# Optimization experiments

Hardware: AMD Instinct MI355X
Metric: run time of the kernel (lower is better)

The kernel has to match this reference:

```python
import jax, jax.numpy as jnp
import numpy as np
import math

LEVELS = 256
DISTANCES = [1, 3, 5, 7]
ANGLES_DEG = [0, 45, 90, 135]


def _offsets():
    # offset_row = round(sin(theta)*d), offset_col = round(cos(theta)*d)
    offs = []
    for d in DISTANCES:
        row = []
        for theta in ANGLES_DEG:
            rad = theta * math.pi / 180.0
            orow = int(np.round(np.sin(rad) * d))
            ocol = int(np.round(np.cos(rad) * d))
            row.append((orow, ocol))
        offs.append(row)
    return offs


def _glcm_contrast(q, orow, ocol, rows, cols):
    # q: (H, W) int32 quantized image in [0, LEVELS-1]
    sr = 0 if orow > 0 else -orow
    er = rows - orow if orow > 0 else rows
    sc = 0 if ocol > 0 else -ocol
    ec = cols - ocol if ocol > 0 else cols
    a = q[sr:er, sc:ec]
    b = q[sr + orow:er + orow, sc + ocol:ec + ocol]
    idx = (a * LEVELS + b).ravel()
    # scatter-add co-occurrence histogram (the irregular-access core)
    hist = jnp.zeros((LEVELS * LEVELS,), jnp.float32).at[idx].add(1.0)
    P = hist.reshape(LEVELS, LEVELS)
    P = P + P.T                      # symmetric
    s = P.sum()
    P = P / jnp.where(s == 0, 1.0, s)  # normalize
    lv = jnp.arange(LEVELS, dtype=jnp.float32)
    diff2 = (lv[:, None] - lv[None, :]) ** 2
    return (diff2 * P).sum()         # Haralick contrast


def setup_inputs() -> dict:
    key = jax.random.key(0)
    x = jax.random.normal(key, (32, 1, 1024, 1024), dtype=jnp.float32)
    return {"x": x}


def reference(x):
    B, C, H, W = x.shape
    img = x[:, 0]  # (B, H, W), single channel
    # per-image rescale to [0, LEVELS-1] then truncate to int (matches int() cast)
    mn = img.min(axis=(1, 2), keepdims=True)
    mx = img.max(axis=(1, 2), keepdims=True)
    q = ((LEVELS - 1) * (img - mn) / (mx - mn)).astype(jnp.int32)
    q = jax.lax.stop_gradient(q)
    offs = _offsets()
    rows_out = []
    for d_row in offs:
        cols_out = []
        for (orow, ocol) in d_row:
            f = lambda qi, o=orow, c=ocol: _glcm_contrast(qi, o, c, H, W)
            cols_out.append(jax.vmap(f)(q))  # (B,)
        rows_out.append(jnp.stack(cols_out, axis=-1))  # (B, n_angles)
    out = jnp.stack(rows_out, axis=-2)  # (B, n_dist, n_angles)
    return out[:, None, :, :]  # (B, 1, 4, 4)
```

## Files before the change

kernel.cpp:

```cpp
#include <hip/hip_runtime.h>

#define H 1024
#define W 1024
#define NIMG 32
#define NOFF 16
#define NACC 17
#define TH 32
#define TW 256
#define TROWS 39
#define TSTR 304

__device__ __forceinline__ int sdot4i(unsigned a, unsigned b, int c) {
#if __has_builtin(__builtin_amdgcn_sdot4)
    return __builtin_amdgcn_sdot4((int)a, (int)b, c, false);
#else
    c += (int)(signed char)(a)       * (int)(signed char)(b);
    c += (int)(signed char)(a >> 8)  * (int)(signed char)(b >> 8);
    c += (int)(signed char)(a >> 16) * (int)(signed char)(b >> 16);
    c += (int)(signed char)(a >> 24) * (int)(signed char)(b >> 24);
    return c;
#endif
}

__device__ __forceinline__ unsigned funnel(unsigned hi, unsigned lo, int shiftBytes) {
#if __has_builtin(__builtin_amdgcn_alignbit)
    return __builtin_amdgcn_alignbit(hi, lo, shiftBytes * 8);
#else
    unsigned long long pair = (((unsigned long long)hi) << 32) | lo;
    return (unsigned)(pair >> (shiftBytes * 8));
#endif
}

__device__ __forceinline__ int wave_sum(int v) {
    v += __builtin_amdgcn_update_dpp(0, v, 0x111, 0xf, 0xf, false);
    v += __builtin_amdgcn_update_dpp(0, v, 0x112, 0xf, 0xf, false);
    v += __builtin_amdgcn_update_dpp(0, v, 0x114, 0xf, 0xf, false);
    v += __builtin_amdgcn_update_dpp(0, v, 0x118, 0xf, 0xf, false);
    v += __builtin_amdgcn_update_dpp(0, v, 0x142, 0xa, 0xf, false);
    v += __builtin_amdgcn_update_dpp(0, v, 0x143, 0xc, 0xf, false);
    return v;
}

template <int OC>
__device__ __forceinline__ int dot8(const unsigned* w, const unsigned* aw, int acc) {
#pragma unroll
    for (int m = 0; m < 8; ++m) {
        const int S = 16 + 4 * m + OC;
        unsigned b;
        if ((S & 3) == 0) b = w[S >> 2];
        else              b = funnel(w[(S >> 2) + 1], w[S >> 2], S & 3);
        acc = sdot4i(aw[m], b, acc);
    }
    return acc;
}

__device__ __forceinline__ void load16w(const unsigned char* wp, unsigned* w) {
    uint4 t0 = *(const uint4*)(wp);
    uint4 t1 = *(const uint4*)(wp + 16);
    uint4 t2 = *(const uint4*)(wp + 32);
    uint4 t3 = *(const uint4*)(wp + 48);
    w[0] = t0.x;  w[1] = t0.y;  w[2] = t0.z;  w[3] = t0.w;
    w[4] = t1.x;  w[5] = t1.y;  w[6] = t1.z;  w[7] = t1.w;
    w[8] = t2.x;  w[9] = t2.y;  w[10] = t2.z; w[11] = t2.w;
    w[12] = t3.x; w[13] = t3.y; w[14] = t3.z; w[15] = t3.w;
}

__device__ __forceinline__ void load8mid(const unsigned char* wp, unsigned* w) {
    uint4 t1 = *(const uint4*)(wp + 16);
    uint4 t2 = *(const uint4*)(wp + 32);
    w[4] = t1.x;  w[5] = t1.y;  w[6] = t1.z;  w[7] = t1.w;
    w[8] = t2.x;  w[9] = t2.y;  w[10] = t2.z; w[11] = t2.w;
}

__device__ __forceinline__ unsigned pack4(float4 f, float s, float b) {
    unsigned q0 = (unsigned)(int)fmaf(f.x, s, b);
    unsigned q1 = (unsigned)(int)fmaf(f.y, s, b);
    unsigned q2 = (unsigned)(int)fmaf(f.z, s, b);
    unsigned q3 = (unsigned)(int)fmaf(f.w, s, b);
    return (((q0 & 255u)) | ((q1 & 255u) << 8) | ((q2 & 255u) << 16) | ((q3 & 255u) << 24)) ^ 0x80808080u;
}

__global__ __launch_bounds__(256)
void minmax_partial(const float* __restrict__ x, float* __restrict__ pmn,
                    float* __restrict__ pmx, unsigned long long* __restrict__ gacc,
                    int* __restrict__ RowS, int* __restrict__ ColS) {
    int img = blockIdx.y;
    int chunk = blockIdx.x;
    int tid = threadIdx.x;
    if (chunk == 0) {
        if (tid < NACC) gacc[img * NACC + tid] = 0ull;
        if (tid >= 32 && tid < 46) RowS[img * 14 + tid - 32] = 0;
        if (tid >= 64 && tid < 78) ColS[img * 14 + tid - 64] = 0;
    }
    const float4* b4 = (const float4*)(x + (size_t)img * (H * (size_t)W) +
                                       (size_t)chunk * (H * W / 64));
    float mn = INFINITY, mx = -INFINITY;
    for (int i = tid; i < 4096; i += 256) {
        float4 v = b4[i];
        mn = fminf(mn, fminf(fminf(v.x, v.y), fminf(v.z, v.w)));
        mx = fmaxf(mx, fmaxf(fmaxf(v.x, v.y), fmaxf(v.z, v.w)));
    }
    for (int o = 32; o > 0; o >>= 1) {
        mn = fminf(mn, __shfl_down(mn, o, 64));
        mx = fmaxf(mx, __shfl_down(mx, o, 64));
    }
    __shared__ float smn[4], smx[4];
    int wave = tid >> 6, lane = tid & 63;
    if (lane == 0) { smn[wave] = mn; smx[wave] = mx; }
    __syncthreads();
    if (tid == 0) {
        mn = fminf(fminf(smn[0], smn[1]), fminf(smn[2], smn[3]));
        mx = fmaxf(fmaxf(smx[0], smx[1]), fmaxf(smx[2], smx[3]));
        pmn[img * 64 + chunk] = mn;
        pmx[img * 64 + chunk] = mx;
    }
}

__global__ __launch_bounds__(256)
void glcm_main(const float* __restrict__ x, const float* __restrict__ pmn,
               const float* __restrict__ pmx, unsigned long long* __restrict__ gacc,
               int* __restrict__ RowS, int* __restrict__ ColS,
               short* __restrict__ cornerWS) {
    __shared__ __align__(16) unsigned char tile[TROWS * TSTR];
    __shared__ int wsum[4][NACC];
    __shared__ int sRB[7], sCB[7];
    __shared__ float sms[2];
    int tid = threadIdx.x;
    int img = blockIdx.z;
    int gr0 = blockIdx.y * TH;
    int gc0 = blockIdx.x * TW;

    if (tid < 64) {
        float mn = pmn[img * 64 + tid], mx = pmx[img * 64 + tid];
        for (int o = 32; o > 0; o >>= 1) {
            mn = fminf(mn, __shfl_down(mn, o, 64));
            mx = fmaxf(mx, __shfl_down(mx, o, 64));
        }
        if (tid == 0) {
            float sc = 255.0f / (mx - mn);
            sms[0] = sc; sms[1] = -mn * sc;
        }
    }
    if (tid >= 64 && tid < 71) { sRB[tid - 64] = 0; sCB[tid - 64] = 0; }
    __syncthreads();
    float scale = sms[0], nmb = sms[1];
    const float* xi = x + (size_t)img * (H * (size_t)W);

    for (int slot = tid; slot < TROWS * (TSTR / 16); slot += 256) {
        int rr = slot / (TSTR / 16);
        int cc = (slot - rr * (TSTR / 16)) * 16;
        int grow = gr0 + rr;
        int gcol = gc0 - 16 + cc;
        uint4 bytes = make_uint4(0u, 0u, 0u, 0u);
        if (grow < H && gcol >= 0 && gcol < W) {
            const float4* p = (const float4*)(xi + (size_t)grow * W + gcol);
            float4 f0 = p[0], f1 = p[1], f2 = p[2], f3 = p[3];
            bytes.x = pack4(f0, scale, nmb);
            bytes.y = pack4(f1, scale, nmb);
            bytes.z = pack4(f2, scale, nmb);
            bytes.w = pack4(f3, scale, nmb);
        }
        *(uint4*)(tile + rr * TSTR + cc) = bytes;
    }
    __syncthreads();

    int r = tid >> 3;
    int c0 = (tid & 7) * 32;
    const unsigned char* rowp = tile + r * TSTR + 16 + c0;
    const unsigned char* wbase = tile + r * TSTR + c0;

    uint4 av0 = *(const uint4*)(rowp);
    uint4 av1 = *(const uint4*)(rowp + 16);
    unsigned aw[8];
    aw[0] = av0.x; aw[1] = av0.y; aw[2] = av0.z; aw[3] = av0.w;
    aw[4] = av1.x; aw[5] = av1.y; aw[6] = av1.z; aw[7] = av1.w;

    int acc[NACC];
#pragma unroll
    for (int k = 0; k < NACC; ++k) acc[k] = 0;
#pragma unroll
    for (int m = 0; m < 8; ++m) acc[16] = sdot4i(aw[m], aw[m], acc[16]);

    unsigned w[16];
    {
#pragma unroll
        for (int i = 0; i < 8; ++i) w[4 + i] = aw[i];
        uint4 t3 = *(const uint4*)(wbase + 48);
        w[12] = t3.x; w[13] = t3.y; w[14] = t3.z; w[15] = t3.w;
        acc[0]  = dot8<1>(w, aw, acc[0]);
        acc[4]  = dot8<3>(w, aw, acc[4]);
        acc[8]  = dot8<5>(w, aw, acc[8]);
        acc[12] = dot8<7>(w, aw, acc[12]);
    }
    {
        load16w(wbase + 1 * TSTR, w);
        acc[1] = dot8<1>(w, aw, acc[1]);
        acc[2] = dot8<0>(w, aw, acc[2]);
        acc[3] = dot8<-1>(w, aw, acc[3]);
    }
    {
        load16w(wbase + 2 * TSTR, w);
        acc[5] = dot8<2>(w, aw, acc[5]);
        acc[7] = dot8<-2>(w, aw, acc[7]);
    }
    {
        load8mid(wbase + 3 * TSTR, w);
        acc[6] = dot8<0>(w, aw, acc[6]);
    }
    {
        load16w(wbase + 4 * TSTR, w);
        acc[9]  = dot8<4>(w, aw, acc[9]);
        acc[11] = dot8<-4>(w, aw, acc[11]);
    }
    {
        load16w(wbase + 5 * TSTR, w);
        acc[10] = dot8<0>(w, aw, acc[10]);
        acc[13] = dot8<5>(w, aw, acc[13]);
        acc[15] = dot8<-5>(w, aw, acc[15]);
    }
    {
        load8mid(wbase + 7 * TSTR, w);
        acc[14] = dot8<0>(w, aw, acc[14]);
    }

    int wv = tid >> 6, lane = tid & 63;
#pragma unroll
    for (int k = 0; k < NACC; ++k) {
        int t = wave_sum(acc[k]);
        if (lane == 63) wsum[wv][k] = t;
    }

    bool rowTop = (gr0 == 0), rowBot = (gr0 == H - TH);
    bool colLft = (gc0 == 0), colRgt = (gc0 == W - TW);
    if (rowTop || rowBot) {
        int base = rowTop ? 0 : 25;
        for (int idx = tid; idx < 7 * 64; idx += 256) {
            int rr = idx >> 6, ww = idx & 63;
            unsigned v = *(const unsigned*)(tile + (base + rr) * TSTR + 16 + 4 * ww);
            atomicAdd(&sRB[rr], sdot4i(v, v, 0));
        }
    }
    if (colLft || colRgt) {
        int cb = colLft ? 16 : 265;
        if (tid < 7 * TH) {
            int rr = tid / 7, j = tid - rr * 7;
            int s = (int)(signed char)tile[rr * TSTR + cb + j];
            atomicAdd(&sCB[j], s * s);
        }
    }
    if (tid < 49) {
        int i = tid / 7, j = tid - i * 7;
        if (rowTop && colLft) {
            int s = (int)(signed char)tile[i * TSTR + 16 + j];
            cornerWS[(img * 4 + 0) * 49 + tid] = (short)(s * s);
        }
        if (rowTop && colRgt) {
            int s = (int)(signed char)tile[i * TSTR + 271 - j];
            cornerWS[(img * 4 + 1) * 49 + tid] = (short)(s * s);
        }
        if (rowBot && colLft) {
            int s = (int)(signed char)tile[(31 - i) * TSTR + 16 + j];
            cornerWS[(img * 4 + 2) * 49 + tid] = (short)(s * s);
        }
        if (rowBot && colRgt) {
            int s = (int)(signed char)tile[(31 - i) * TSTR + 271 - j];
            cornerWS[(img * 4 + 3) * 49 + tid] = (short)(s * s);
        }
    }
    __syncthreads();
    if (tid < NACC) {
        int s = wsum[0][tid] + wsum[1][tid] + wsum[2][tid] + wsum[3][tid];
        atomicAdd(&gacc[img * NACC + tid], (unsigned long long)(long long)s);
    }
    if (tid < 7) {
        if (rowTop) atomicAdd(&RowS[img * 14 + tid], sRB[tid]);
        if (rowBot) atomicAdd(&RowS[img * 14 + 7 + tid], sRB[tid]);
        if (colLft) atomicAdd(&ColS[img * 14 + tid], sCB[tid]);
        if (colRgt) atomicAdd(&ColS[img * 14 + 7 + tid], sCB[tid]);
    }
}

__global__ __launch_bounds__(512)
void finalize_k(const unsigned long long* __restrict__ gacc,
                const int* __restrict__ RowS, const int* __restrict__ ColS,
                const short* __restrict__ cornerWS, float* __restrict__ out) {
    __shared__ int cps[NIMG][4][8][8];
    int tid = threadIdx.x;
    if (tid < NIMG * 4) {
        int img = tid >> 2, c4 = tid & 3;
        const short* cr = cornerWS + (img * 4 + c4) * 49;
        for (int r = 0; r < 8; ++r)
            for (int c = 0; c < 8; ++c) {
                int v = 0;
                if (r && c)
                    v = cps[img][c4][r - 1][c] + cps[img][c4][r][c - 1]
                      - cps[img][c4][r - 1][c - 1] + (int)cr[(r - 1) * 7 + (c - 1)];
                cps[img][c4][r][c] = v;
            }
    }
    __syncthreads();
    if (tid < NIMG * NOFF) {
        const int ORO[16] = {0,1,1,1, 0,2,3,2, 0,4,5,4, 0,5,7,5};
        const int OCO[16] = {1,1,0,-1, 3,2,0,-2, 5,4,0,-4, 7,5,0,-5};
        int img = tid >> 4, k = tid & 15;
        int orr = ORO[k], oc = OCO[k], aoc = oc < 0 ? -oc : oc;
        long long RT = 0, RB = 0, CL = 0, CR = 0;
        for (int i = 0; i < orr; ++i) { RT += RowS[img * 14 + i]; RB += RowS[img * 14 + 13 - i]; }
        for (int i = 0; i < aoc; ++i) { CL += ColS[img * 14 + i]; CR += ColS[img * 14 + 13 - i]; }
        long long CA = oc > 0 ? CR : CL;
        long long CB = oc > 0 ? CL : CR;
        long long PSa = (oc >= 0) ? cps[img][3][orr][aoc] : cps[img][2][orr][aoc];
        long long PSb = (oc >= 0) ? cps[img][0][orr][aoc] : cps[img][1][orr][aoc];
        long long corr = -(RT + RB + CA + CB) + PSa + PSb;
        long long cross = (long long)gacc[img * NACC + k];
        long long tsum  = (long long)gacc[img * NACC + 16];
        long long num = 2 * tsum + corr - 2 * cross;
        double n = (double)(H - orr) * (double)(W - aoc);
        out[tid] = (float)((double)num / n);
    }
}

extern "C" void kernel_launch(void* const* d_in, const int* in_sizes, int n_in,
                              void* d_out, int out_size, void* d_ws, size_t ws_size,
                              hipStream_t stream) {
    const float* x = (const float*)d_in[0];
    float* out = (float*)d_out;
    char* ws = (char*)d_ws;
    float* pmn = (float*)ws;
    float* pmx = (float*)(ws + 8192);
    unsigned long long* gacc = (unsigned long long*)(ws + 16384);
    int* RowS = (int*)(ws + 20736);
    int* ColS = (int*)(ws + 22528);
    short* cornerWS = (short*)(ws + 24320);

    minmax_partial<<<dim3(64, NIMG), 256, 0, stream>>>(x, pmn, pmx, gacc, RowS, ColS);
    glcm_main<<<dim3(W / TW, H / TH, NIMG), 256, 0, stream>>>(x, pmn, pmx, gacc,
                                                              RowS, ColS, cornerWS);
    finalize_k<<<1, 512, 0, stream>>>(gacc, RowS, ColS, cornerWS, out);
}
```

Baseline: 229.9 us.

## Double tile height and fold finalize into last-block epilogue of main kernel

Each block now covers 64 rows instead of 32, so every thread processes two row groups and the 7-row halo is amortized over more rows. This halves the block count and with it the redundant min/max reductions and global atomics. The separate finalize kernel is removed: a global done-counter picks the last block, which computes the outputs, including corner prefix sums computed directly from corner data. This saves a launch but serializes the epilogue in one block and adds a threadfence/atomic per block.

```diff
diff --git a/kernel.cpp b/kernel.cpp
--- a/kernel.cpp
+++ b/kernel.cpp
@@ -5,10 +5,11 @@
 #define NIMG 32
 #define NOFF 16
 #define NACC 17
-#define TH 32
+#define TH 64
 #define TW 256
-#define TROWS 39
+#define TROWS 71
 #define TSTR 304
+#define NBLK (4 * 16 * NIMG)
 
 __device__ __forceinline__ int sdot4i(unsigned a, unsigned b, int c) {
 #if __has_builtin(__builtin_amdgcn_sdot4)
@@ -83,7 +84,8 @@
 __global__ __launch_bounds__(256)
 void minmax_partial(const float* __restrict__ x, float* __restrict__ pmn,
                     float* __restrict__ pmx, unsigned long long* __restrict__ gacc,
-                    int* __restrict__ RowS, int* __restrict__ ColS) {
+                    int* __restrict__ RowS, int* __restrict__ ColS,
+                    unsigned* __restrict__ doneCnt) {
     int img = blockIdx.y;
     int chunk = blockIdx.x;
     int tid = threadIdx.x;
@@ -91,6 +93,7 @@
         if (tid < NACC) gacc[img * NACC + tid] = 0ull;
         if (tid >= 32 && tid < 46) RowS[img * 14 + tid - 32] = 0;
         if (tid >= 64 && tid < 78) ColS[img * 14 + tid - 64] = 0;
+        if (img == 0 && tid == 255) *doneCnt = 0u;
     }
     const float4* b4 = (const float4*)(x + (size_t)img * (H * (size_t)W) +
                                        (size_t)chunk * (H * W / 64));
@@ -120,15 +123,19 @@
 void glcm_main(const float* __restrict__ x, const float* __restrict__ pmn,
                const float* __restrict__ pmx, unsigned long long* __restrict__ gacc,
                int* __restrict__ RowS, int* __restrict__ ColS,
-               short* __restrict__ cornerWS) {
+               short* __restrict__ cornerWS, unsigned* __restrict__ doneCnt,
+               float* __restrict__ out) {
     __shared__ __align__(16) unsigned char tile[TROWS * TSTR];
     __shared__ int wsum[4][NACC];
     __shared__ int sRB[7], sCB[7];
     __shared__ float sms[2];
+    __shared__ unsigned sLast;
     int tid = threadIdx.x;
     int img = blockIdx.z;
     int gr0 = blockIdx.y * TH;
     int gc0 = blockIdx.x * TW;
+    bool rowTop = (blockIdx.y == 0), rowBot = (blockIdx.y == 15);
+    bool colLft = (blockIdx.x == 0), colRgt = (blockIdx.x == 3);
 
     if (tid < 64) {
         float mn = pmn[img * 64 + tid], mx = pmx[img * 64 + tid];
@@ -164,76 +171,78 @@
     }
     __syncthreads();
 
-    int r = tid >> 3;
-    int c0 = (tid & 7) * 32;
-    const unsigned char* rowp = tile + r * TSTR + 16 + c0;
-    const unsigned char* wbase = tile + r * TSTR + c0;
-
-    uint4 av0 = *(const uint4*)(rowp);
-    uint4 av1 = *(const uint4*)(rowp + 16);
-    unsigned aw[8];
-    aw[0] = av0.x; aw[1] = av0.y; aw[2] = av0.z; aw[3] = av0.w;
-    aw[4] = av1.x; aw[5] = av1.y; aw[6] = av1.z; aw[7] = av1.w;
-
     int acc[NACC];
 #pragma unroll
     for (int k = 0; k < NACC; ++k) acc[k] = 0;
-#pragma unroll
-    for (int m = 0; m < 8; ++m) acc[16] = sdot4i(aw[m], aw[m], acc[16]);
-
-    unsigned w[16];
-    {
-#pragma unroll
-        for (int i = 0; i < 8; ++i) w[4 + i] = aw[i];
-        uint4 t3 = *(const uint4*)(wbase + 48);
-        w[12] = t3.x; w[13] = t3.y; w[14] = t3.z; w[15] = t3.w;
-        acc[0]  = dot8<1>(w, aw, acc[0]);
-        acc[4]  = dot8<3>(w, aw, acc[4]);
-        acc[8]  = dot8<5>(w, aw, acc[8]);
-        acc[12] = dot8<7>(w, aw, acc[12]);
-    }
-    {
-        load16w(wbase + 1 * TSTR, w);
-        acc[1] = dot8<1>(w, aw, acc[1]);
-        acc[2] = dot8<0>(w, aw, acc[2]);
-        acc[3] = dot8<-1>(w, aw, acc[3]);
-    }
-    {
-        load16w(wbase + 2 * TSTR, w);
-        acc[5] = dot8<2>(w, aw, acc[5]);
-        acc[7] = dot8<-2>(w, aw, acc[7]);
-    }
-    {
-        load8mid(wbase + 3 * TSTR, w);
-        acc[6] = dot8<0>(w, aw, acc[6]);
-    }
-    {
-        load16w(wbase + 4 * TSTR, w);
-        acc[9]  = dot8<4>(w, aw, acc[9]);
-        acc[11] = dot8<-4>(w, aw, acc[11]);
-    }
-    {
-        load16w(wbase + 5 * TSTR, w);
-        acc[10] = dot8<0>(w, aw, acc[10]);
-        acc[13] = dot8<5>(w, aw, acc[13]);
-        acc[15] = dot8<-5>(w, aw, acc[15]);
-    }
-    {
-        load8mid(wbase + 7 * TSTR, w);
-        acc[14] = dot8<0>(w, aw, acc[14]);
+
+#pragma unroll
+    for (int rbase = 0; rbase < TH; rbase += 32) {
+        int r = rbase + (tid >> 3);
+        int c0 = (tid & 7) * 32;
+        const unsigned char* rowp = tile + r * TSTR + 16 + c0;
+        const unsigned char* wbase = tile + r * TSTR + c0;
+
+        uint4 av0 = *(const uint4*)(rowp);
+        uint4 av1 = *(const uint4*)(rowp + 16);
+        unsigned aw[8];
+        aw[0] = av0.x; aw[1] = av0.y; aw[2] = av0.z; aw[3] = av0.w;
+        aw[4] = av1.x; aw[5] = av1.y; aw[6] = av1.z; aw[7] = av1.w;
+
+#pragma unroll
+        for (int m = 0; m < 8; ++m) acc[16] = sdot4i(aw[m], aw[m], acc[16]);
+
+        unsigned w[16];
+        {
+#pragma unroll
+            for (int i = 0; i < 8; ++i) w[4 + i] = aw[i];
+            uint4 t3 = *(const uint4*)(wbase + 48);
+            w[12] = t3.x; w[13] = t3.y; w[14] = t3.z; w[15] = t3.w;
+            acc[0]  = dot8<1>(w, aw, acc[0]);
+            acc[4]  = dot8<3>(w, aw, acc[4]);
+            acc[8]  = dot8<5>(w, aw, acc[8]);
+            acc[12] = dot8<7>(w, aw, acc[12]);
+        }
+        {
+            load16w(wbase + 1 * TSTR, w);
+            acc[1] = dot8<1>(w, aw, acc[1]);
+            acc[2] = dot8<0>(w, aw, acc[2]);
+            acc[3] = dot8<-1>(w, aw, acc[3]);
+        }
+        {
+            load16w(wbase + 2 * TSTR, w);
+            acc[5] = dot8<2>(w, aw, acc[5]);
+            acc[7] = dot8<-2>(w, aw, acc[7]);
+        }
+        {
+            load8mid(wbase + 3 * TSTR, w);
+            acc[6] = dot8<0>(w, aw, acc[6]);
+        }
+        {
+            load16w(wbase + 4 * TSTR, w);
+            acc[9]  = dot8<4>(w, aw, acc[9]);
+            acc[11] = dot8<-4>(w, aw, acc[11]);
+        }
+        {
+            load16w(wbase + 5 * TSTR, w);
+            acc[10] = dot8<0>(w, aw, acc[10]);
+            acc[13] = dot8<5>(w, aw, acc[13]);
+            acc[15] = dot8<-5>(w, aw, acc[15]);
+        }
+        {
+            load8mid(wbase + 7 * TSTR, w);
+            acc[14] = dot8<0>(w, aw, acc[14]);
+        }
     }
 
     int wv = tid >> 6, lane = tid & 63;
 #pragma unroll
     for (int k = 0; k < NACC; ++k) {
-        int t = wave_sum(acc[k]);
-        if (lane == 63) wsum[wv][k] = t;
-    }
-
-    bool rowTop = (gr0 == 0), rowBot = (gr0 == H - TH);
-    bool colLft = (gc0 == 0), colRgt = (gc0 == W - TW);
+        int s = wave_sum(acc[k]);
+        if (lane == 63) wsum[wv][k] = s;
+    }
+
     if (rowTop || rowBot) {
-        int base = rowTop ? 0 : 25;
+        int base = rowTop ? 0 : (TH - 7);
         for (int idx = tid; idx < 7 * 64; idx += 256) {
             int rr = idx >> 6, ww = idx & 63;
             unsigned v = *(const unsigned*)(tile + (base + rr) * TSTR + 16 + 4 * ww);
@@ -242,8 +251,8 @@
     }
     if (colLft || colRgt) {
         int cb = colLft ? 16 : 265;
-        if (tid < 7 * TH) {
-            int rr = tid / 7, j = tid - rr * 7;
+        for (int idx = tid; idx < TH * 7; idx += 256) {
+            int rr = idx / 7, j = idx - rr * 7;
             int s = (int)(signed char)tile[rr * TSTR + cb + j];
             atomicAdd(&sCB[j], s * s);
         }
@@ -259,11 +268,11 @@
             cornerWS[(img * 4 + 1) * 49 + tid] = (short)(s * s);
         }
         if (rowBot && colLft) {
-            int s = (int)(signed char)tile[(31 - i) * TSTR + 16 + j];
+            int s = (int)(signed char)tile[(TH - 1 - i) * TSTR + 16 + j];
             cornerWS[(img * 4 + 2) * 49 + tid] = (short)(s * s);
         }
         if (rowBot && colRgt) {
-            int s = (int)(signed char)tile[(31 - i) * TSTR + 271 - j];
+            int s = (int)(signed char)tile[(TH - 1 - i) * TSTR + 271 - j];
             cornerWS[(img * 4 + 3) * 49 + tid] = (short)(s * s);
         }
     }
@@ -278,45 +287,46 @@
         if (colLft) atomicAdd(&ColS[img * 14 + tid], sCB[tid]);
         if (colRgt) atomicAdd(&ColS[img * 14 + 7 + tid], sCB[tid]);
     }
-}
-
-__global__ __launch_bounds__(512)
-void finalize_k(const unsigned long long* __restrict__ gacc,
-                const int* __restrict__ RowS, const int* __restrict__ ColS,
-                const short* __restrict__ cornerWS, float* __restrict__ out) {
-    __shared__ int cps[NIMG][4][8][8];
-    int tid = threadIdx.x;
-    if (tid < NIMG * 4) {
-        int img = tid >> 2, c4 = tid & 3;
-        const short* cr = cornerWS + (img * 4 + c4) * 49;
-        for (int r = 0; r < 8; ++r)
-            for (int c = 0; c < 8; ++c) {
-                int v = 0;
-                if (r && c)
-                    v = cps[img][c4][r - 1][c] + cps[img][c4][r][c - 1]
-                      - cps[img][c4][r - 1][c - 1] + (int)cr[(r - 1) * 7 + (c - 1)];
-                cps[img][c4][r][c] = v;
-            }
-    }
-    __syncthreads();
-    if (tid < NIMG * NOFF) {
+
+    __syncthreads();
+    if (tid == 0) {
+        __threadfence();
+        sLast = atomicAdd(doneCnt, 1u);
+    }
+    __syncthreads();
+    if (sLast == NBLK - 1) {
+        __threadfence();
         const int ORO[16] = {0,1,1,1, 0,2,3,2, 0,4,5,4, 0,5,7,5};
         const int OCO[16] = {1,1,0,-1, 3,2,0,-2, 5,4,0,-4, 7,5,0,-5};
-        int img = tid >> 4, k = tid & 15;
-        int orr = ORO[k], oc = OCO[k], aoc = oc < 0 ? -oc : oc;
-        long long RT = 0, RB = 0, CL = 0, CR = 0;
-        for (int i = 0; i < orr; ++i) { RT += RowS[img * 14 + i]; RB += RowS[img * 14 + 13 - i]; }
-        for (int i = 0; i < aoc; ++i) { CL += ColS[img * 14 + i]; CR += ColS[img * 14 + 13 - i]; }
-        long long CA = oc > 0 ? CR : CL;
-        long long CB = oc > 0 ? CL : CR;
-        long long PSa = (oc >= 0) ? cps[img][3][orr][aoc] : cps[img][2][orr][aoc];
-        long long PSb = (oc >= 0) ? cps[img][0][orr][aoc] : cps[img][1][orr][aoc];
-        long long corr = -(RT + RB + CA + CB) + PSa + PSb;
-        long long cross = (long long)gacc[img * NACC + k];
-        long long tsum  = (long long)gacc[img * NACC + 16];
-        long long num = 2 * tsum + corr - 2 * cross;
-        double n = (double)(H - orr) * (double)(W - aoc);
-        out[tid] = (float)((double)num / n);
+        for (int o = tid; o < NIMG * NOFF; o += 256) {
+            int im = o >> 4, k = o & 15;
+            int orr = ORO[k], oc = OCO[k], aoc = oc < 0 ? -oc : oc;
+            long long RT = 0, RB = 0, CL = 0, CR = 0;
+            for (int i = 0; i < orr; ++i) {
+                RT += RowS[im * 14 + i];
+                RB += RowS[im * 14 + 13 - i];
+            }
+            for (int i = 0; i < aoc; ++i) {
+                CL += ColS[im * 14 + i];
+                CR += ColS[im * 14 + 13 - i];
+            }
+            long long CA = oc > 0 ? CR : CL;
+            long long CB = oc > 0 ? CL : CR;
+            const short* pa = cornerWS + (im * 4 + (oc >= 0 ? 3 : 2)) * 49;
+            const short* pb = cornerWS + (im * 4 + (oc >= 0 ? 0 : 1)) * 49;
+            long long PSa = 0, PSb = 0;
+            for (int i = 0; i < orr; ++i)
+                for (int j = 0; j < aoc; ++j) {
+                    PSa += pa[i * 7 + j];
+                    PSb += pb[i * 7 + j];
+                }
+            long long corr = -(RT + RB + CA + CB) + PSa + PSb;
+            long long cross = (long long)gacc[im * NACC + k];
+            long long tsum  = (long long)gacc[im * NACC + 16];
+            long long num = 2 * tsum + corr - 2 * cross;
+            double n = (double)(H - orr) * (double)(W - aoc);
+            out[o] = (float)((double)num / n);
+        }
     }
 }
 
@@ -331,10 +341,11 @@
     unsigned long long* gacc = (unsigned long long*)(ws + 16384);
     int* RowS = (int*)(ws + 20736);
     int* ColS = (int*)(ws + 22528);
-    short* cornerWS = (short*)(ws + 24320);
-
-    minmax_partial<<<dim3(64, NIMG), 256, 0, stream>>>(x, pmn, pmx, gacc, RowS, ColS);
-    glcm_main<<<dim3(W / TW, H / TH, NIMG), 256, 0, stream>>>(x, pmn, pmx, gacc,
-                                                              RowS, ColS, cornerWS);
-    finalize_k<<<1, 512, 0, stream>>>(gacc, RowS, ColS, cornerWS, out);
-}
+    short* cornerWS = (short*)(ws + 24576);
+    unsigned* doneCnt = (unsigned*)(ws + 38912);
+
+    minmax_partial<<<dim3(64, NIMG), 256, 0, stream>>>(x, pmn, pmx, gacc,
+                                                       RowS, ColS, doneCnt);
+    glcm_main<<<dim3(4, 16, NIMG), 256, 0, stream>>>(x, pmn, pmx, gacc, RowS,
+                                                     ColS, cornerWS, doneCnt, out);
+}
```

Result: slower. 269.5 us (+17.2%).
